# Kernel optimization log

Measured on AMD Instinct MI355X. Metric: run time of the kernel, lower is better.

The kernel has to match this reference:

```python
import jax, jax.numpy as jnp
import numpy as np


def setup_inputs() -> dict:
    key = jax.random.key(0)
    k1, k2, k3, k4 = jax.random.split(key, 4)
    B, Sq, Sk, d = 16, 2048, 2048, 64
    queries = jax.random.normal(k1, (B, Sq, d), dtype=jnp.float32)
    keys = jax.random.normal(k2, (B, Sk, d), dtype=jnp.float32)
    values = jax.random.normal(k3, (B, Sk, d), dtype=jnp.float32)
    # True = padded key position (masked out)
    key_padding_mask = jax.random.randint(k4, (B, Sk), 0, 2) == 1
    return {"queries": queries, "keys": keys, "values": values,
            "key_padding_mask": key_padding_mask}


def reference(queries, keys, values, key_padding_mask):
    d = queries.shape[-1]
    # scores: [B, Sq, Sk]
    scores = jnp.einsum("bqd,bkd->bqk", queries, keys) / jnp.sqrt(
        jnp.asarray(d, dtype=queries.dtype))
    # padded keys get -inf before softmax (mask broadcast over query dim)
    scores = jnp.where(key_padding_mask[:, None, :], -jnp.inf, scores)
    attention_weights = jax.nn.softmax(scores, axis=2)
    return jnp.einsum("bqk,bkd->bqd", attention_weights, values)
```

## Files before the change

kernel.cpp:

```cpp
#include <hip/hip_runtime.h>
#include <hip/hip_bf16.h>

#define NB 16
#define SQ 2048
#define SK 2048
#define DH 64

#define KBLK 1024
#define VBLK 512
#define BBLK 128

typedef __attribute__((ext_vector_type(8))) short short8;
typedef __attribute__((ext_vector_type(8))) __bf16 bf16x8;
typedef __attribute__((ext_vector_type(4))) float floatx4;
typedef __attribute__((ext_vector_type(16))) float floatx16;
typedef __attribute__((ext_vector_type(2))) unsigned uint2v;

__device__ __forceinline__ unsigned pk2(float a, float b) {
  __hip_bfloat162 h = __float22bfloat162_rn(make_float2(a, b));
  unsigned u; __builtin_memcpy(&u, &h, 4); return u;
}
__device__ __forceinline__ floatx16 mfma32(short8 a, short8 b, floatx16 c) {
  return __builtin_amdgcn_mfma_f32_32x32x16_bf16(
      __builtin_bit_cast(bf16x8, a), __builtin_bit_cast(bf16x8, b), c, 0, 0, 0);
}

__global__ __launch_bounds__(256)
void prepass(const float* __restrict__ K, const float* __restrict__ V,
             const int* __restrict__ m, short* __restrict__ Kb,
             short* __restrict__ Vt, float* __restrict__ bias) {
  __shared__ unsigned tlw[64 * 33];
  const int blk = blockIdx.x;
  const int t = threadIdx.x;
  if (blk < KBLK) {
    size_t i8 = ((size_t)blk * 256 + t) * 8;
    floatx4 a = *(const floatx4*)(K + i8);
    floatx4 b = *(const floatx4*)(K + i8 + 4);
    union { unsigned u[4]; short8 s; } w;
    w.u[0] = pk2(a[0], a[1]); w.u[1] = pk2(a[2], a[3]);
    w.u[2] = pk2(b[0], b[1]); w.u[3] = pk2(b[2], b[3]);
    *(short8*)(Kb + i8) = w.s;
  } else if (blk < KBLK + VBLK) {
    const int bt = blk - KBLK;
    const int key2 = t & 31;
    const int dg = (t >> 5) * 8;
    const float* vp0 = V + ((size_t)bt * 64 + 2 * key2) * 64 + dg;
    const float* vp1 = vp0 + 64;
    floatx4 va  = *(const floatx4*)(vp0);
    floatx4 va2 = *(const floatx4*)(vp0 + 4);
    floatx4 vb  = *(const floatx4*)(vp1);
    floatx4 vb2 = *(const floatx4*)(vp1 + 4);
#pragma unroll
    for (int j = 0; j < 4; ++j) {
      tlw[(dg + j) * 33 + key2]     = pk2(va[j],  vb[j]);
      tlw[(dg + 4 + j) * 33 + key2] = pk2(va2[j], vb2[j]);
    }
    __syncthreads();
    const short* tls = (const short*)tlw;
    short* dst = Vt + (size_t)bt * 4096;
#pragma unroll
    for (int i = 0; i < 2; ++i) {
      int idx = i * 2048 + t * 8;
      int d = idx >> 6, key = idx & 63;
      *(short8*)(dst + idx) = *(const short8*)(tls + d * 66 + key);
    }
  } else {
    int i = (blk - KBLK - VBLK) * 256 + t;
    bias[i] = m[i] ? -1e30f : 0.0f;
  }
}

__global__ __launch_bounds__(256)
void attn_main(const float* __restrict__ Q, const short* __restrict__ Kb,
               const short* __restrict__ Vt, const float* __restrict__ bias,
               float* __restrict__ Out, float* __restrict__ Op1,
               float2* __restrict__ ml) {
  __shared__ __align__(16) short ks[64 * 64];
  __shared__ __align__(16) short vt[64 * 64];
  __shared__ __align__(16) short pb[4 * 32 * 64];

  const int half = blockIdx.x >> 8;
  const int rest = blockIdx.x & 255;
  const int b    = rest >> 4;
  const int qt   = rest & 15;
  const int tid  = threadIdx.x;
  const int wave = tid >> 6;
  const int lane = tid & 63;
  const int n32  = lane & 31;
  const int h    = lane >> 5;
  const int sw   = n32 & 7;
  const int q0   = qt * 128 + wave * 32;
  const int kt0  = half << 4;

  const float QS = 0.125f * 1.4426950408889634f;
  short8 qf[4];
  {
    const float* qp = Q + ((size_t)b * SQ + q0 + n32) * DH + 8 * h;
#pragma unroll
    for (int c = 0; c < 4; ++c) {
      floatx4 a  = *(const floatx4*)(qp + 16 * c);
      floatx4 a2 = *(const floatx4*)(qp + 16 * c + 4);
      union { unsigned u[4]; short8 s; } w;
      w.u[0] = pk2(a[0] * QS, a[1] * QS);
      w.u[1] = pk2(a[2] * QS, a[3] * QS);
      w.u[2] = pk2(a2[0] * QS, a2[1] * QS);
      w.u[3] = pk2(a2[2] * QS, a2[3] * QS);
      qf[c] = w.s;
    }
  }

  floatx16 o0, o1;
#pragma unroll
  for (int i = 0; i < 16; ++i) { o0[i] = 0.f; o1[i] = 0.f; }
  float m_q = -1e30f, l_q = 0.f;

  short* pw = pb + wave * 2048;

  const short* kg = Kb + (size_t)b * SK * DH;
  const short* vg = Vt + (size_t)b * 32 * 4096;
  const float* bg = bias + b * SK;

  const int srow  = tid >> 3;
  const int schk  = tid & 7;
  const int sphys = schk ^ (srow & 7);
  const int soff0 = srow * 64 + sphys * 8;
  const int soff1 = (srow + 32) * 64 + sphys * 8;
  const int goff0 = srow * 64 + schk * 8;
  const int goff1 = (srow + 32) * 64 + schk * 8;

  short8 kr[2], vr[2];
  {
    const short* kn = kg + (size_t)kt0 * 4096;
    const short* vn = vg + (size_t)kt0 * 4096;
    kr[0] = *(const short8*)(kn + goff0); kr[1] = *(const short8*)(kn + goff1);
    vr[0] = *(const short8*)(vn + goff0); vr[1] = *(const short8*)(vn + goff1);
  }

  for (int kt = kt0; kt < kt0 + 16; ++kt) {
    *(short8*)(ks + soff0) = kr[0]; *(short8*)(ks + soff1) = kr[1];
    *(short8*)(vt + soff0) = vr[0]; *(short8*)(vt + soff1) = vr[1];
    __syncthreads();

    if (kt + 1 < kt0 + 16) {
      const short* kn = kg + (size_t)(kt + 1) * 4096;
      const short* vn = vg + (size_t)(kt + 1) * 4096;
      kr[0] = *(const short8*)(kn + goff0); kr[1] = *(const short8*)(kn + goff1);
      vr[0] = *(const short8*)(vn + goff0); vr[1] = *(const short8*)(vn + goff1);
    }

    floatx16 s0, s1;
#pragma unroll
    for (int i = 0; i < 16; ++i) { s0[i] = 0.f; s1[i] = 0.f; }
#pragma unroll
    for (int c = 0; c < 4; ++c) {
      short8 kf0 = *(short8*)(ks + n32 * 64        + ((2 * c + h) ^ sw) * 8);
      short8 kf1 = *(short8*)(ks + (32 + n32) * 64 + ((2 * c + h) ^ sw) * 8);
      s0 = mfma32(kf0, qf[c], s0);
      s1 = mfma32(kf1, qf[c], s1);
    }

    const float* bq = bg + kt * 64;
    float sc0[16], sc1[16];
    float rm = -1e30f;
#pragma unroll
    for (int u = 0; u < 4; ++u) {
      floatx4 bv0 = *(const floatx4*)(bq + 8 * u + 4 * h);
      floatx4 bv1 = *(const floatx4*)(bq + 32 + 8 * u + 4 * h);
#pragma unroll
      for (int i = 0; i < 4; ++i) {
        sc0[4 * u + i] = s0[4 * u + i] + bv0[i];
        sc1[4 * u + i] = s1[4 * u + i] + bv1[i];
        rm = fmaxf(rm, fmaxf(sc0[4 * u + i], sc1[4 * u + i]));
      }
    }
    rm = fmaxf(rm, __shfl_xor(rm, 32));
    float mn = fmaxf(m_q, rm);
    float alpha = __builtin_amdgcn_exp2f(m_q - mn);
    bool up = mn > m_q;
    m_q = mn;

    float rs = 0.f;
#pragma unroll
    for (int u = 0; u < 4; ++u) {
      float p0 = __builtin_amdgcn_exp2f(sc0[4 * u + 0] - mn);
      float p1 = __builtin_amdgcn_exp2f(sc0[4 * u + 1] - mn);
      float p2 = __builtin_amdgcn_exp2f(sc0[4 * u + 2] - mn);
      float p3 = __builtin_amdgcn_exp2f(sc0[4 * u + 3] - mn);
      rs += (p0 + p1) + (p2 + p3);
      uint2v w; w.x = pk2(p0, p1); w.y = pk2(p2, p3);
      *(uint2v*)(pw + n32 * 64 + (u ^ sw) * 8 + 4 * h) = w;

      float q0v = __builtin_amdgcn_exp2f(sc1[4 * u + 0] - mn);
      float q1v = __builtin_amdgcn_exp2f(sc1[4 * u + 1] - mn);
      float q2v = __builtin_amdgcn_exp2f(sc1[4 * u + 2] - mn);
      float q3v = __builtin_amdgcn_exp2f(sc1[4 * u + 3] - mn);
      rs += (q0v + q1v) + (q2v + q3v);
      uint2v w2; w2.x = pk2(q0v, q1v); w2.y = pk2(q2v, q3v);
      *(uint2v*)(pw + n32 * 64 + ((4 + u) ^ sw) * 8 + 4 * h) = w2;
    }
    rs += __shfl_xor(rs, 32);
    l_q = alpha * l_q + rs;

    if (__ballot(up)) {
#pragma unroll
      for (int i = 0; i < 16; ++i) { o0[i] *= alpha; o1[i] *= alpha; }
    }

#pragma unroll
    for (int c = 0; c < 4; ++c) {
      short8 pf  = *(short8*)(pw + n32 * 64 + ((2 * c + h) ^ sw) * 8);
      short8 vf0 = *(short8*)(vt + n32 * 64        + ((2 * c + h) ^ sw) * 8);
      short8 vf1 = *(short8*)(vt + (32 + n32) * 64 + ((2 * c + h) ^ sw) * 8);
      o0 = mfma32(vf0, pf, o0);
      o1 = mfma32(vf1, pf, o1);
    }
    __syncthreads();
  }

  float* Od = half ? Op1 : Out;
  float* orow = Od + ((size_t)b * SQ + q0 + n32) * DH;
#pragma unroll
  for (int u = 0; u < 4; ++u) {
    floatx4 w0, w1;
#pragma unroll
    for (int i = 0; i < 4; ++i) { w0[i] = o0[4 * u + i]; w1[i] = o1[4 * u + i]; }
    *(floatx4*)(orow + 8 * u + 4 * h)      = w0;
    *(floatx4*)(orow + 32 + 8 * u + 4 * h) = w1;
  }
  if (lane < 32)
    ml[(size_t)half * NB * SQ + (size_t)b * SQ + q0 + lane] = make_float2(m_q, l_q);
}

__global__ __launch_bounds__(256)
void combine(const float* __restrict__ Op1, const float2* __restrict__ ml,
             float* __restrict__ Out) {
  int idx = blockIdx.x * 256 + threadIdx.x;
  int q = idx >> 3;
  int dc = (idx & 7) * 8;
  float2 s0 = ml[q];
  float2 s1 = ml[NB * SQ + q];
  float M = fmaxf(s0.x, s1.x);
  float w0 = __builtin_amdgcn_exp2f(s0.x - M);
  float w1 = __builtin_amdgcn_exp2f(s1.x - M);
  float inv = 1.0f / (s0.y * w0 + s1.y * w1);
  const float* p0 = Out + (size_t)q * DH + dc;
  const float* p1 = Op1 + (size_t)q * DH + dc;
  floatx4 a0 = *(const floatx4*)(p0);
  floatx4 a1 = *(const floatx4*)(p0 + 4);
  floatx4 b0 = *(const floatx4*)(p1);
  floatx4 b1 = *(const floatx4*)(p1 + 4);
  floatx4 r0 = (a0 * w0 + b0 * w1) * inv;
  floatx4 r1 = (a1 * w0 + b1 * w1) * inv;
  *(floatx4*)(Out + (size_t)q * DH + dc) = r0;
  *(floatx4*)(Out + (size_t)q * DH + dc + 4) = r1;
}

extern "C" void kernel_launch(void* const* d_in, const int* in_sizes, int n_in,
                              void* d_out, int out_size, void* d_ws, size_t ws_size,
                              hipStream_t stream) {
  const float* Q = (const float*)d_in[0];
  const float* K = (const float*)d_in[1];
  const float* V = (const float*)d_in[2];
  const int* mask = (const int*)d_in[3];
  float* Out = (float*)d_out;

  char* ws = (char*)d_ws;
  short*  Kb   = (short*)(ws);
  short*  Vt   = (short*)(ws + 4194304);
  float*  bias = (float*)(ws + 8388608);
  float2* ml   = (float2*)(ws + 8519680);
  float*  Op1  = (float*)(ws + 9043968);

  prepass  <<<KBLK + VBLK + BBLK, 256, 0, stream>>>(K, V, mask, Kb, Vt, bias);
  attn_main<<<2 * NB * (SQ / 128), 256, 0, stream>>>(Q, Kb, Vt, bias, Out, Op1, ml);
  combine  <<<NB * SQ * DH / 8 / 256, 256, 0, stream>>>(Op1, ml, Out);
}
```

Baseline: 121.1 us.

## Drop LDS staging: load K/V fragments directly from global and shuffle P in registers

Removes the shared-memory tiles for K, V and P along with both per-iteration block barriers. Each wave now loads its MFMA K and V fragments straight from global memory (K prefetched one tile ahead) and builds the P operand with cross-half lane shuffles instead of an LDS round trip. Launch bounds now ask for two blocks per SU. The trade is redundant global/L2 traffic: the four waves of a block each read the same K/V tile, and register pressure rises.

```diff
diff --git a/kernel.cpp b/kernel.cpp
--- a/kernel.cpp
+++ b/kernel.cpp
@@ -70,15 +70,11 @@
   }
 }
 
-__global__ __launch_bounds__(256)
+__global__ __launch_bounds__(256, 2)
 void attn_main(const float* __restrict__ Q, const short* __restrict__ Kb,
                const short* __restrict__ Vt, const float* __restrict__ bias,
                float* __restrict__ Out, float* __restrict__ Op1,
                float2* __restrict__ ml) {
-  __shared__ __align__(16) short ks[64 * 64];
-  __shared__ __align__(16) short vt[64 * 64];
-  __shared__ __align__(16) short pb[4 * 32 * 64];
-
   const int half = blockIdx.x >> 8;
   const int rest = blockIdx.x & 255;
   const int b    = rest >> 4;
@@ -88,7 +84,6 @@
   const int lane = tid & 63;
   const int n32  = lane & 31;
   const int h    = lane >> 5;
-  const int sw   = n32 & 7;
   const int q0   = qt * 128 + wave * 32;
   const int kt0  = half << 4;
 
@@ -114,63 +109,51 @@
   for (int i = 0; i < 16; ++i) { o0[i] = 0.f; o1[i] = 0.f; }
   float m_q = -1e30f, l_q = 0.f;
 
-  short* pw = pb + wave * 2048;
-
-  const short* kg = Kb + (size_t)b * SK * DH;
-  const short* vg = Vt + (size_t)b * 32 * 4096;
-  const float* bg = bias + b * SK;
-
-  const int srow  = tid >> 3;
-  const int schk  = tid & 7;
-  const int sphys = schk ^ (srow & 7);
-  const int soff0 = srow * 64 + sphys * 8;
-  const int soff1 = (srow + 32) * 64 + sphys * 8;
-  const int goff0 = srow * 64 + schk * 8;
-  const int goff1 = (srow + 32) * 64 + schk * 8;
-
-  short8 kr[2], vr[2];
-  {
-    const short* kn = kg + (size_t)kt0 * 4096;
-    const short* vn = vg + (size_t)kt0 * 4096;
-    kr[0] = *(const short8*)(kn + goff0); kr[1] = *(const short8*)(kn + goff1);
-    vr[0] = *(const short8*)(vn + goff0); vr[1] = *(const short8*)(vn + goff1);
+  const short* kg = Kb + (size_t)b * SK * DH + (size_t)n32 * 64 + 8 * h;
+  const short* vg = Vt + (size_t)b * 32 * 4096 + (size_t)n32 * 64 + 8 * h;
+  const float* bg = bias + b * SK + 4 * h;
+
+  short8 kf[8];
+#pragma unroll
+  for (int c = 0; c < 4; ++c) {
+    kf[2 * c]     = *(const short8*)(kg + (size_t)kt0 * 4096 + 16 * c);
+    kf[2 * c + 1] = *(const short8*)(kg + (size_t)kt0 * 4096 + 2048 + 16 * c);
   }
 
   for (int kt = kt0; kt < kt0 + 16; ++kt) {
-    *(short8*)(ks + soff0) = kr[0]; *(short8*)(ks + soff1) = kr[1];
-    *(short8*)(vt + soff0) = vr[0]; *(short8*)(vt + soff1) = vr[1];
-    __syncthreads();
-
-    if (kt + 1 < kt0 + 16) {
-      const short* kn = kg + (size_t)(kt + 1) * 4096;
-      const short* vn = vg + (size_t)(kt + 1) * 4096;
-      kr[0] = *(const short8*)(kn + goff0); kr[1] = *(const short8*)(kn + goff1);
-      vr[0] = *(const short8*)(vn + goff0); vr[1] = *(const short8*)(vn + goff1);
-    }
-
     floatx16 s0, s1;
 #pragma unroll
     for (int i = 0; i < 16; ++i) { s0[i] = 0.f; s1[i] = 0.f; }
 #pragma unroll
     for (int c = 0; c < 4; ++c) {
-      short8 kf0 = *(short8*)(ks + n32 * 64        + ((2 * c + h) ^ sw) * 8);
-      short8 kf1 = *(short8*)(ks + (32 + n32) * 64 + ((2 * c + h) ^ sw) * 8);
-      s0 = mfma32(kf0, qf[c], s0);
-      s1 = mfma32(kf1, qf[c], s1);
+      s0 = mfma32(kf[2 * c], qf[c], s0);
+      s1 = mfma32(kf[2 * c + 1], qf[c], s1);
+    }
+
+    short8 vf[8];
+#pragma unroll
+    for (int c = 0; c < 4; ++c) {
+      vf[2 * c]     = *(const short8*)(vg + (size_t)kt * 4096 + 16 * c);
+      vf[2 * c + 1] = *(const short8*)(vg + (size_t)kt * 4096 + 2048 + 16 * c);
+    }
+    const int ktn = (kt + 1 < kt0 + 16) ? kt + 1 : kt;
+#pragma unroll
+    for (int c = 0; c < 4; ++c) {
+      kf[2 * c]     = *(const short8*)(kg + (size_t)ktn * 4096 + 16 * c);
+      kf[2 * c + 1] = *(const short8*)(kg + (size_t)ktn * 4096 + 2048 + 16 * c);
     }
 
     const float* bq = bg + kt * 64;
-    float sc0[16], sc1[16];
     float rm = -1e30f;
 #pragma unroll
     for (int u = 0; u < 4; ++u) {
-      floatx4 bv0 = *(const floatx4*)(bq + 8 * u + 4 * h);
-      floatx4 bv1 = *(const floatx4*)(bq + 32 + 8 * u + 4 * h);
+      floatx4 bv0 = *(const floatx4*)(bq + 8 * u);
+      floatx4 bv1 = *(const floatx4*)(bq + 32 + 8 * u);
 #pragma unroll
       for (int i = 0; i < 4; ++i) {
-        sc0[4 * u + i] = s0[4 * u + i] + bv0[i];
-        sc1[4 * u + i] = s1[4 * u + i] + bv1[i];
-        rm = fmaxf(rm, fmaxf(sc0[4 * u + i], sc1[4 * u + i]));
+        s0[4 * u + i] += bv0[i];
+        s1[4 * u + i] += bv1[i];
+        rm = fmaxf(rm, fmaxf(s0[4 * u + i], s1[4 * u + i]));
       }
     }
     rm = fmaxf(rm, __shfl_xor(rm, 32));
@@ -179,24 +162,21 @@
     bool up = mn > m_q;
     m_q = mn;
 
+    uint2v pka[4], pkb[4];
     float rs = 0.f;
 #pragma unroll
     for (int u = 0; u < 4; ++u) {
-      float p0 = __builtin_amdgcn_exp2f(sc0[4 * u + 0] - mn);
-      float p1 = __builtin_amdgcn_exp2f(sc0[4 * u + 1] - mn);
-      float p2 = __builtin_amdgcn_exp2f(sc0[4 * u + 2] - mn);
-      float p3 = __builtin_amdgcn_exp2f(sc0[4 * u + 3] - mn);
-      rs += (p0 + p1) + (p2 + p3);
-      uint2v w; w.x = pk2(p0, p1); w.y = pk2(p2, p3);
-      *(uint2v*)(pw + n32 * 64 + (u ^ sw) * 8 + 4 * h) = w;
-
-      float q0v = __builtin_amdgcn_exp2f(sc1[4 * u + 0] - mn);
-      float q1v = __builtin_amdgcn_exp2f(sc1[4 * u + 1] - mn);
-      float q2v = __builtin_amdgcn_exp2f(sc1[4 * u + 2] - mn);
-      float q3v = __builtin_amdgcn_exp2f(sc1[4 * u + 3] - mn);
-      rs += (q0v + q1v) + (q2v + q3v);
-      uint2v w2; w2.x = pk2(q0v, q1v); w2.y = pk2(q2v, q3v);
-      *(uint2v*)(pw + n32 * 64 + ((4 + u) ^ sw) * 8 + 4 * h) = w2;
+      float p0 = __builtin_amdgcn_exp2f(s0[4 * u + 0] - mn);
+      float p1 = __builtin_amdgcn_exp2f(s0[4 * u + 1] - mn);
+      float p2 = __builtin_amdgcn_exp2f(s0[4 * u + 2] - mn);
+      float p3 = __builtin_amdgcn_exp2f(s0[4 * u + 3] - mn);
+      float r0 = __builtin_amdgcn_exp2f(s1[4 * u + 0] - mn);
+      float r1 = __builtin_amdgcn_exp2f(s1[4 * u + 1] - mn);
+      float r2 = __builtin_amdgcn_exp2f(s1[4 * u + 2] - mn);
+      float r3 = __builtin_amdgcn_exp2f(s1[4 * u + 3] - mn);
+      rs += ((p0 + p1) + (p2 + p3)) + ((r0 + r1) + (r2 + r3));
+      pka[u].x = pk2(p0, p1); pka[u].y = pk2(p2, p3);
+      pkb[u].x = pk2(r0, r1); pkb[u].y = pk2(r2, r3);
     }
     rs += __shfl_xor(rs, 32);
     l_q = alpha * l_q + rs;
@@ -208,13 +188,20 @@
 
 #pragma unroll
     for (int c = 0; c < 4; ++c) {
-      short8 pf  = *(short8*)(pw + n32 * 64 + ((2 * c + h) ^ sw) * 8);
-      short8 vf0 = *(short8*)(vt + n32 * 64        + ((2 * c + h) ^ sw) * 8);
-      short8 vf1 = *(short8*)(vt + (32 + n32) * 64 + ((2 * c + h) ^ sw) * 8);
-      o0 = mfma32(vf0, pf, o0);
-      o1 = mfma32(vf1, pf, o1);
-    }
-    __syncthreads();
+      uint2v blo = (c < 2) ? pka[2 * (c & 1)]     : pkb[2 * (c & 1)];
+      uint2v bhi = (c < 2) ? pka[2 * (c & 1) + 1] : pkb[2 * (c & 1) + 1];
+      uint2v own  = h ? bhi : blo;
+      uint2v send = h ? blo : bhi;
+      uint2v recv;
+      recv.x = (unsigned)__shfl_xor((int)send.x, 32);
+      recv.y = (unsigned)__shfl_xor((int)send.y, 32);
+      uint2v lo = h ? recv : own;
+      uint2v hi = h ? own : recv;
+      union { unsigned u[4]; short8 s; } pf;
+      pf.u[0] = lo.x; pf.u[1] = lo.y; pf.u[2] = hi.x; pf.u[3] = hi.y;
+      o0 = mfma32(vf[2 * c], pf.s, o0);
+      o1 = mfma32(vf[2 * c + 1], pf.s, o1);
+    }
   }
 
   float* Od = half ? Op1 : Out;
```

Result: slower. 152.1 us (+25.7%).
